# Kernel optimization log

Hardware: AMD Instinct MI355X
Metric: run time of the kernel (lower is better)

## Reference

```python
import jax, jax.numpy as jnp
import numpy as np

B, C, D = 4, 512, 1024
N = 8           # num_experts
DFF = 4096      # GEGLU inner dim; in-projection outputs 2*DFF


def setup_inputs() -> dict:
    key = jax.random.key(0)
    ks = jax.random.split(key, 7)
    hidden_states = jax.random.normal(ks[0], (B, C, D), dtype=jnp.float32)
    # Dispatch mask: one-hot expert assignment per token (top-1 routing).
    assign = jax.random.randint(ks[1], (B, C), 0, N)
    dispatch_mask = jax.nn.one_hot(assign, N, dtype=jnp.float32)        # [B,C,N]
    # Combine mask: same sparsity pattern, scaled by a router probability.
    probs = jax.random.uniform(ks[2], (B, C, 1), dtype=jnp.float32)
    combine_mask = dispatch_mask * probs                                 # [B,C,N]
    s_in = 1.0 / np.sqrt(D)
    s_out = 1.0 / np.sqrt(DFF)
    W_in = jax.random.normal(ks[3], (N, 2 * DFF, D), dtype=jnp.float32) * s_in
    b_in = jax.random.normal(ks[4], (N, 2 * DFF), dtype=jnp.float32) * 0.01
    W_out = jax.random.normal(ks[5], (N, D, DFF), dtype=jnp.float32) * s_out
    b_out = jax.random.normal(ks[6], (N, D), dtype=jnp.float32) * 0.01
    return {"hidden_states": hidden_states, "dispatch_mask": dispatch_mask,
            "combine_mask": combine_mask, "W_in": W_in, "b_in": b_in,
            "W_out": W_out, "b_out": b_out}


def reference(hidden_states, dispatch_mask, combine_mask, W_in, b_in, W_out, b_out):
    # Dispatch: [B,C,D] x [B,C,N] -> [N,B,C,D]
    h = jnp.einsum('bcd,bcn->nbcd', hidden_states, dispatch_mask)
    # Per-expert GEGLU FFN.
    h = jnp.einsum('nbcd,nfd->nbcf', h, W_in) + b_in[:, None, None, :]   # [N,B,C,2*DFF]
    x, gate = jnp.split(h, 2, axis=-1)
    h = x * jax.nn.gelu(gate, approximate=False)                          # torch F.gelu = exact erf
    h = jnp.einsum('nbcd,nfd->nbcf', h, W_out) + b_out[:, None, None, :]  # [N,B,C,D]
    # Combine: [N,B,C,D] x [B,C,N] -> [B,C,D]
    return jnp.einsum('nbcd,bcn->bcd', h, combine_mask)
```

## Files before the change

kernel.cpp:

```cpp
#include <hip/hip_runtime.h>
#include <math.h>

#define NTOK 2048
#define DDIM 1024
#define NEXP 8
#define DFF 4096
#define TWODFF 8192

typedef __attribute__((ext_vector_type(8))) short bf16x8;
typedef __attribute__((ext_vector_type(4))) float f32x4;

__device__ __forceinline__ short f2bf(float f) {
  unsigned u = __builtin_bit_cast(unsigned, f);
  u = (u + 0x7FFFu + ((u >> 16) & 1u)) >> 16;
  return (short)u;
}

__device__ __forceinline__ unsigned pk2(float a, float b) {
  unsigned r;
  asm("v_cvt_pk_bf16_f32 %0, %1, %2" : "=v"(r) : "v"(a), "v"(b));
  return r;
}

__global__ void route_k(const float* __restrict__ disp, const float* __restrict__ comb,
                        int* __restrict__ cnt, int* __restrict__ tokl,
                        float* __restrict__ scale) {
  __shared__ int lcnt[NEXP];
  const int tid = threadIdx.x;
  if (tid < NEXP) lcnt[tid] = 0;
  __syncthreads();
  for (int i = 0; i < 8; ++i) {
    const int t = i * 256 + tid;
    const float* row = disp + (size_t)t * NEXP;
    int e = 0;
#pragma unroll
    for (int n = 1; n < NEXP; ++n) e = (row[n] > row[e]) ? n : e;
    const float p = comb[(size_t)t * NEXP + e];
    const int slot = atomicAdd(&lcnt[e], 1);
    tokl[e * NTOK + slot] = t;
    scale[t] = p;
  }
  __syncthreads();
  if (tid < NEXP) cnt[tid] = lcnt[tid];
}

#define G1_LOAD(aR, bR, k0) do {                                              \
  _Pragma("unroll") for (int i_ = 0; i_ < 4; ++i_) {                          \
    bR[i_] = *(const float4*)(bP[i_] + (k0));                                 \
    aR[i_] = aP[i_] ? *(const float4*)(aP[i_] + (k0))                         \
                    : make_float4(0.f, 0.f, 0.f, 0.f);                        \
  } } while (0)

#define G1_STORE(aR, bR, buf) do {                                            \
  _Pragma("unroll") for (int i_ = 0; i_ < 4; ++i_) {                          \
    const int row_ = i_ * 32 + r0;                                            \
    const int ba_ = (row_ * 64 + (tid & 7) * 8) ^ ((row_ & 7) << 4);          \
    uint2 va_, vb_;                                                           \
    va_.x = pk2(aR[i_].x, aR[i_].y); va_.y = pk2(aR[i_].z, aR[i_].w);         \
    vb_.x = pk2(bR[i_].x, bR[i_].y); vb_.y = pk2(bR[i_].z, bR[i_].w);         \
    *(uint2*)((char*)Al[buf] + ba_) = va_;                                    \
    *(uint2*)((char*)Bl[buf] + ba_) = vb_;                                    \
  } } while (0)

__global__ __launch_bounds__(256, 2) void gemm1_k(
    const float* __restrict__ hid, const float* __restrict__ Win,
    const float* __restrict__ bin, const int* __restrict__ cnt,
    const int* __restrict__ tokl, short* __restrict__ act) {
  const int e = blockIdx.z;
  const int Me = cnt[e];
  const int m0 = blockIdx.y * 128;
  if (m0 >= Me) return;
  const int f0 = blockIdx.x * 64;

  __shared__ short Al[3][128 * 32];
  __shared__ short Bl[3][128 * 32];
  __shared__ int tokids[128];

  const int tid = threadIdx.x;
  if (tid < 128) {
    const int r = m0 + tid;
    tokids[tid] = (r < Me) ? tokl[e * NTOK + r] : -1;
  }
  __syncthreads();

  const int r0 = tid >> 3;
  const int c0 = (tid & 7) * 4;
  const float* aP[4];
  const float* bP[4];
#pragma unroll
  for (int i = 0; i < 4; ++i) {
    const int row = i * 32 + r0;
    const int tk = tokids[row];
    aP[i] = (tk >= 0) ? (hid + (size_t)tk * DDIM + c0) : nullptr;
    const int wr = (row < 64) ? (f0 + row) : (DFF + f0 + (row - 64));
    bP[i] = Win + (size_t)e * TWODFF * DDIM + (size_t)wr * DDIM + c0;
  }

  const int wid = tid >> 6, lane = tid & 63;
  const int wm = (wid >> 1) * 64;
  const int wf = (wid & 1) * 32;
  const int lr = lane & 15;
  const int kbyte = (lane >> 4) * 16;

  f32x4 accx[4][2], accg[4][2];
  const f32x4 zf = {0.f, 0.f, 0.f, 0.f};
#pragma unroll
  for (int a = 0; a < 4; ++a)
#pragma unroll
    for (int b = 0; b < 2; ++b) { accx[a][b] = zf; accg[a][b] = zf; }

  float4 aRa[4], bRa[4], aRb[4], bRb[4];
  G1_LOAD(aRa, bRa, 0);
  G1_STORE(aRa, bRa, 0);
  G1_LOAD(aRa, bRa, 32);
  G1_LOAD(aRb, bRb, 64);

  for (int kt = 0; kt < 32; ++kt) {
    __syncthreads();
    const char* Ab = (const char*)Al[kt % 3];
    const char* Bb = (const char*)Bl[kt % 3];
    bf16x8 a[4], bx[2], bg[2];
#pragma unroll
    for (int fm = 0; fm < 4; ++fm) {
      const int row = wm + fm * 16 + lr;
      a[fm] = *(const bf16x8*)(Ab + ((row * 64 + kbyte) ^ ((row & 7) << 4)));
    }
#pragma unroll
    for (int ff = 0; ff < 2; ++ff) {
      const int rx = wf + ff * 16 + lr;
      bx[ff] = *(const bf16x8*)(Bb + ((rx * 64 + kbyte) ^ ((rx & 7) << 4)));
      const int rg = rx + 64;
      bg[ff] = *(const bf16x8*)(Bb + ((rg * 64 + kbyte) ^ ((rg & 7) << 4)));
    }
#pragma unroll
    for (int fm = 0; fm < 4; ++fm)
#pragma unroll
      for (int ff = 0; ff < 2; ++ff) {
        accx[fm][ff] = __builtin_amdgcn_mfma_f32_16x16x32_bf16(a[fm], bx[ff], accx[fm][ff], 0, 0, 0);
        accg[fm][ff] = __builtin_amdgcn_mfma_f32_16x16x32_bf16(a[fm], bg[ff], accg[fm][ff], 0, 0, 0);
      }
    if (kt < 31) {
      const int wb = (kt + 1) % 3;
      if (kt & 1) {
        G1_STORE(aRb, bRb, wb);
        if (kt < 29) G1_LOAD(aRb, bRb, (kt + 3) * 32);
      } else {
        G1_STORE(aRa, bRa, wb);
        if (kt < 29) G1_LOAD(aRa, bRa, (kt + 3) * 32);
      }
    }
  }

  const int orb = (lane >> 4) * 4;
#pragma unroll
  for (int ff = 0; ff < 2; ++ff) {
    const int fcol = f0 + wf + ff * 16 + lr;
    const float bx_ = bin[e * TWODFF + fcol];
    const float bg_ = bin[e * TWODFF + DFF + fcol];
#pragma unroll
    for (int fm = 0; fm < 4; ++fm)
#pragma unroll
      for (int j = 0; j < 4; ++j) {
        const int row = wm + fm * 16 + orb + j;
        if (m0 + row < Me) {
          const float x = accx[fm][ff][j] + bx_;
          const float g = accg[fm][ff][j] + bg_;
          const float gl = 0.5f * g * (1.f + erff(g * 0.70710678118654752f));
          act[(size_t)tokids[row] * DFF + fcol] = f2bf(x * gl);
        }
      }
  }
}

__global__ __launch_bounds__(256) void gemm2_k(
    const short* __restrict__ act, const float* __restrict__ Wout,
    const float* __restrict__ bout, const int* __restrict__ cnt,
    const int* __restrict__ tokl, const float* __restrict__ scale,
    float* __restrict__ out) {
  const int e = blockIdx.z;
  const int Me = cnt[e];
  const int m0 = blockIdx.y * 128;
  if (m0 >= Me) return;
  const int n0 = blockIdx.x * 64;

  __shared__ short Al[2][128 * 64];
  __shared__ short Bl[2][64 * 64];
  __shared__ int tokids[128];
  __shared__ float pv[128];

  const int tid = threadIdx.x;
  if (tid < 128) {
    const int r = m0 + tid;
    const int tk = (r < Me) ? tokl[e * NTOK + r] : -1;
    tokids[tid] = tk;
    pv[tid] = (tk >= 0) ? scale[tk] : 0.f;
  }
  __syncthreads();

  const int ar0 = tid >> 3;
  const int ac0 = (tid & 7) * 8;
  const short* aP[4];
#pragma unroll
  for (int i = 0; i < 4; ++i) {
    const int row = i * 32 + ar0;
    const int tk = tokids[row];
    aP[i] = (tk >= 0) ? (act + (size_t)tk * DFF + ac0) : nullptr;
  }
  const int br0 = tid >> 4;
  const float* bP[4];
#pragma unroll
  for (int i = 0; i < 4; ++i) {
    const int row = i * 16 + br0;
    bP[i] = Wout + (size_t)e * DDIM * DFF + (size_t)(n0 + row) * DFF + (tid & 15) * 4;
  }

  bf16x8 aR[4];
  float4 bR[4];
  auto load_t = [&](int k0) {
#pragma unroll
    for (int i = 0; i < 4; ++i) bR[i] = *(const float4*)(bP[i] + k0);
    const bf16x8 z = {0, 0, 0, 0, 0, 0, 0, 0};
#pragma unroll
    for (int i = 0; i < 4; ++i) aR[i] = aP[i] ? *(const bf16x8*)(aP[i] + k0) : z;
  };
  auto store_t = [&](int buf) {
#pragma unroll
    for (int i = 0; i < 4; ++i) {
      const int row = i * 32 + ar0;
      const int ba = (row * 128 + (tid & 7) * 16) ^ ((row & 7) << 4);
      *(bf16x8*)((char*)Al[buf] + ba) = aR[i];
    }
#pragma unroll
    for (int i = 0; i < 4; ++i) {
      const int row = i * 16 + br0;
      const int bb = (row * 128 + (tid & 15) * 8) ^ ((row & 7) << 4);
      uint2 vb;
      vb.x = pk2(bR[i].x, bR[i].y); vb.y = pk2(bR[i].z, bR[i].w);
      *(uint2*)((char*)Bl[buf] + bb) = vb;
    }
  };

  const int wid = tid >> 6, lane = tid & 63;
  const int wm = (wid >> 1) * 64;
  const int wn = (wid & 1) * 32;
  const int lr = lane & 15;
  const int lkb = (lane >> 4) * 16;

  f32x4 acc[4][2];
  const f32x4 zf = {0.f, 0.f, 0.f, 0.f};
#pragma unroll
  for (int a = 0; a < 4; ++a) { acc[a][0] = zf; acc[a][1] = zf; }

  load_t(0);
  store_t(0);

  for (int kt = 0; kt < 64; ++kt) {
    if (kt < 63) load_t((kt + 1) * 64);
    __syncthreads();
    const char* Ab = (const char*)Al[kt & 1];
    const char* Bb = (const char*)Bl[kt & 1];
#pragma unroll
    for (int ks = 0; ks < 2; ++ks) {
      bf16x8 a[4], b[2];
      const int kb = ks * 64 + lkb;
#pragma unroll
      for (int fm = 0; fm < 4; ++fm) {
        const int row = wm + fm * 16 + lr;
        a[fm] = *(const bf16x8*)(Ab + ((row * 128 + kb) ^ ((row & 7) << 4)));
      }
#pragma unroll
      for (int ff = 0; ff < 2; ++ff) {
        const int rn = wn + ff * 16 + lr;
        b[ff] = *(const bf16x8*)(Bb + ((rn * 128 + kb) ^ ((rn & 7) << 4)));
      }
#pragma unroll
      for (int fm = 0; fm < 4; ++fm)
#pragma unroll
        for (int ff = 0; ff < 2; ++ff)
          acc[fm][ff] = __builtin_amdgcn_mfma_f32_16x16x32_bf16(a[fm], b[ff], acc[fm][ff], 0, 0, 0);
    }
    if (kt < 63) store_t((kt + 1) & 1);
  }

  const int orb = (lane >> 4) * 4;
#pragma unroll
  for (int ff = 0; ff < 2; ++ff) {
    const int ncol = n0 + wn + ff * 16 + lr;
    const float bo = bout[e * DDIM + ncol];
#pragma unroll
    for (int fm = 0; fm < 4; ++fm)
#pragma unroll
      for (int j = 0; j < 4; ++j) {
        const int row = wm + fm * 16 + orb + j;
        if (m0 + row < Me)
          out[(size_t)tokids[row] * DDIM + ncol] = pv[row] * (acc[fm][ff][j] + bo);
      }
  }
}

extern "C" void kernel_launch(void* const* d_in, const int* in_sizes, int n_in,
                              void* d_out, int out_size, void* d_ws, size_t ws_size,
                              hipStream_t stream) {
  const float* hid = (const float*)d_in[0];
  const float* disp = (const float*)d_in[1];
  const float* comb = (const float*)d_in[2];
  const float* Win = (const float*)d_in[3];
  const float* bin = (const float*)d_in[4];
  const float* Wout = (const float*)d_in[5];
  const float* bout = (const float*)d_in[6];
  float* out = (float*)d_out;

  char* ws = (char*)d_ws;
  int* cnt = (int*)(ws);
  int* tokl = (int*)(ws + 256);
  float* scale = (float*)(ws + 256 + NTOK * NEXP * 4);
  short* act = (short*)(ws + (1 << 17));

  route_k<<<1, 256, 0, stream>>>(disp, comb, cnt, tokl, scale);
  gemm1_k<<<dim3(DFF / 64, 4, NEXP), 256, 0, stream>>>(hid, Win, bin, cnt, tokl, act);
  gemm2_k<<<dim3(DDIM / 64, 4, NEXP), 256, 0, stream>>>(act, Wout, bout, cnt, tokl, scale, out);
}
```

Baseline: 241.5 us.

## Rework GEMM pipelines: double-buffered LDS with two-deep register prefetch

In gemm1 the LDS tiles go from a triple buffer to a double buffer. Global loads for tile kt+2 are now issued right after the barrier, into alternating register sets. In gemm2 the single register stage becomes two alternating register sets that prefetch two tiles ahead, and the kernel gets launch_bounds(256,2). The aim is to hide global latency better, reduce LDS use in gemm1 and raise occupancy in gemm2, at the cost of extra live registers that may cause spills.

```diff
diff --git a/kernel.cpp b/kernel.cpp
--- a/kernel.cpp
+++ b/kernel.cpp
@@ -72,8 +72,8 @@
   if (m0 >= Me) return;
   const int f0 = blockIdx.x * 64;
 
-  __shared__ short Al[3][128 * 32];
-  __shared__ short Bl[3][128 * 32];
+  __shared__ short Al[2][128 * 32];
+  __shared__ short Bl[2][128 * 32];
   __shared__ int tokids[128];
 
   const int tid = threadIdx.x;
@@ -112,13 +112,16 @@
   float4 aRa[4], bRa[4], aRb[4], bRb[4];
   G1_LOAD(aRa, bRa, 0);
   G1_STORE(aRa, bRa, 0);
-  G1_LOAD(aRa, bRa, 32);
-  G1_LOAD(aRb, bRb, 64);
+  G1_LOAD(aRb, bRb, 32);
 
   for (int kt = 0; kt < 32; ++kt) {
     __syncthreads();
-    const char* Ab = (const char*)Al[kt % 3];
-    const char* Bb = (const char*)Bl[kt % 3];
+    if (kt < 30) {
+      if (kt & 1) G1_LOAD(aRb, bRb, (kt + 2) * 32);
+      else        G1_LOAD(aRa, bRa, (kt + 2) * 32);
+    }
+    const char* Ab = (const char*)Al[kt & 1];
+    const char* Bb = (const char*)Bl[kt & 1];
     bf16x8 a[4], bx[2], bg[2];
 #pragma unroll
     for (int fm = 0; fm < 4; ++fm) {
@@ -140,14 +143,8 @@
         accg[fm][ff] = __builtin_amdgcn_mfma_f32_16x16x32_bf16(a[fm], bg[ff], accg[fm][ff], 0, 0, 0);
       }
     if (kt < 31) {
-      const int wb = (kt + 1) % 3;
-      if (kt & 1) {
-        G1_STORE(aRb, bRb, wb);
-        if (kt < 29) G1_LOAD(aRb, bRb, (kt + 3) * 32);
-      } else {
-        G1_STORE(aRa, bRa, wb);
-        if (kt < 29) G1_LOAD(aRa, bRa, (kt + 3) * 32);
-      }
+      if (kt & 1) G1_STORE(aRa, bRa, (kt + 1) & 1);
+      else        G1_STORE(aRb, bRb, (kt + 1) & 1);
     }
   }
 
@@ -172,7 +169,28 @@
   }
 }
 
-__global__ __launch_bounds__(256) void gemm2_k(
+#define G2_LOAD(aR, bR, k0) do {                                              \
+  _Pragma("unroll") for (int i_ = 0; i_ < 4; ++i_)                            \
+    bR[i_] = *(const float4*)(bP[i_] + (k0));                                 \
+  _Pragma("unroll") for (int i_ = 0; i_ < 4; ++i_)                            \
+    aR[i_] = aP[i_] ? *(const bf16x8*)(aP[i_] + (k0)) : zro;                  \
+  } while (0)
+
+#define G2_STORE(aR, bR, buf) do {                                            \
+  _Pragma("unroll") for (int i_ = 0; i_ < 4; ++i_) {                          \
+    const int row_ = i_ * 32 + ar0;                                           \
+    const int ba_ = (row_ * 128 + (tid & 7) * 16) ^ ((row_ & 7) << 4);        \
+    *(bf16x8*)((char*)Al[buf] + ba_) = aR[i_];                                \
+  }                                                                           \
+  _Pragma("unroll") for (int i_ = 0; i_ < 4; ++i_) {                          \
+    const int row_ = i_ * 16 + br0;                                           \
+    const int bb_ = (row_ * 128 + (tid & 15) * 8) ^ ((row_ & 7) << 4);        \
+    uint2 vb_;                                                                \
+    vb_.x = pk2(bR[i_].x, bR[i_].y); vb_.y = pk2(bR[i_].z, bR[i_].w);         \
+    *(uint2*)((char*)Bl[buf] + bb_) = vb_;                                    \
+  } } while (0)
+
+__global__ __launch_bounds__(256, 2) void gemm2_k(
     const short* __restrict__ act, const float* __restrict__ Wout,
     const float* __restrict__ bout, const int* __restrict__ cnt,
     const int* __restrict__ tokl, const float* __restrict__ scale,
@@ -214,32 +232,7 @@
     bP[i] = Wout + (size_t)e * DDIM * DFF + (size_t)(n0 + row) * DFF + (tid & 15) * 4;
   }
 
-  bf16x8 aR[4];
-  float4 bR[4];
-  auto load_t = [&](int k0) {
-#pragma unroll
-    for (int i = 0; i < 4; ++i) bR[i] = *(const float4*)(bP[i] + k0);
-    const bf16x8 z = {0, 0, 0, 0, 0, 0, 0, 0};
-#pragma unroll
-    for (int i = 0; i < 4; ++i) aR[i] = aP[i] ? *(const bf16x8*)(aP[i] + k0) : z;
-  };
-  auto store_t = [&](int buf) {
-#pragma unroll
-    for (int i = 0; i < 4; ++i) {
-      const int row = i * 32 + ar0;
-      const int ba = (row * 128 + (tid & 7) * 16) ^ ((row & 7) << 4);
-      *(bf16x8*)((char*)Al[buf] + ba) = aR[i];
-    }
-#pragma unroll
-    for (int i = 0; i < 4; ++i) {
-      const int row = i * 16 + br0;
-      const int bb = (row * 128 + (tid & 15) * 8) ^ ((row & 7) << 4);
-      uint2 vb;
-      vb.x = pk2(bR[i].x, bR[i].y); vb.y = pk2(bR[i].z, bR[i].w);
-      *(uint2*)((char*)Bl[buf] + bb) = vb;
-    }
-  };
-
+  const bf16x8 zro = {0, 0, 0, 0, 0, 0, 0, 0};
   const int wid = tid >> 6, lane = tid & 63;
   const int wm = (wid >> 1) * 64;
   const int wn = (wid & 1) * 32;
@@ -251,12 +244,18 @@
 #pragma unroll
   for (int a = 0; a < 4; ++a) { acc[a][0] = zf; acc[a][1] = zf; }
 
-  load_t(0);
-  store_t(0);
+  bf16x8 aRa[4], aRb[4];
+  float4 bRa[4], bRb[4];
+  G2_LOAD(aRa, bRa, 0);
+  G2_STORE(aRa, bRa, 0);
+  G2_LOAD(aRb, bRb, 64);
 
   for (int kt = 0; kt < 64; ++kt) {
-    if (kt < 63) load_t((kt + 1) * 64);
     __syncthreads();
+    if (kt < 62) {
+      if (kt & 1) G2_LOAD(aRb, bRb, (kt + 2) * 64);
+      else        G2_LOAD(aRa, bRa, (kt + 2) * 64);
+    }
     const char* Ab = (const char*)Al[kt & 1];
     const char* Bb = (const char*)Bl[kt & 1];
 #pragma unroll
@@ -279,7 +278,10 @@
         for (int ff = 0; ff < 2; ++ff)
           acc[fm][ff] = __builtin_amdgcn_mfma_f32_16x16x32_bf16(a[fm], b[ff], acc[fm][ff], 0, 0, 0);
     }
-    if (kt < 63) store_t((kt + 1) & 1);
+    if (kt < 63) {
+      if (kt & 1) G2_STORE(aRa, bRa, (kt + 1) & 1);
+      else        G2_STORE(aRb, bRb, (kt + 1) & 1);
+    }
   }
 
   const int orb = (lane >> 4) * 4;
```

Result: slower. 260.1 us (+7.7%).

## Switch gemm1 to double-buffered LDS with padded rows and explicit barrier

Applied to the files above, without the earlier changes.

Replaces the triple-buffered, XOR-swizzled LDS staging in the first expert GEMM with two buffers using 80-byte padded rows. Global prefetch is now issued at the start of each iteration, two tiles ahead, and the converted registers are stored after the MFMAs. A custom waitcnt plus s_barrier sits at the end of each iteration instead of __syncthreads at the start. It also drops the min-blocks-per-SM launch bound, which may raise register use and lower occupancy. Padding changes the LDS bank-conflict pattern compared with the swizzle.

```diff
diff --git a/kernel.cpp b/kernel.cpp
--- a/kernel.cpp
+++ b/kernel.cpp
@@ -20,6 +20,11 @@
   unsigned r;
   asm("v_cvt_pk_bf16_f32 %0, %1, %2" : "=v"(r) : "v"(a), "v"(b));
   return r;
+}
+
+__device__ __forceinline__ void ldsbar() {
+  asm volatile("s_waitcnt lgkmcnt(0)" ::: "memory");
+  __builtin_amdgcn_s_barrier();
 }
 
 __global__ void route_k(const float* __restrict__ disp, const float* __restrict__ comb,
@@ -44,25 +49,25 @@
   if (tid < NEXP) cnt[tid] = lcnt[tid];
 }
 
-#define G1_LOAD(aR, bR, k0) do {                                              \
+#define G1_LOAD(sa, sb, k0) do {                                              \
   _Pragma("unroll") for (int i_ = 0; i_ < 4; ++i_) {                          \
-    bR[i_] = *(const float4*)(bP[i_] + (k0));                                 \
-    aR[i_] = aP[i_] ? *(const float4*)(aP[i_] + (k0))                         \
+    sb[i_] = *(const float4*)(bP[i_] + (k0));                                 \
+    sa[i_] = aP[i_] ? *(const float4*)(aP[i_] + (k0))                         \
                     : make_float4(0.f, 0.f, 0.f, 0.f);                        \
   } } while (0)
 
-#define G1_STORE(aR, bR, buf) do {                                            \
+#define G1_STORE(sa, sb, buf) do {                                            \
   _Pragma("unroll") for (int i_ = 0; i_ < 4; ++i_) {                          \
     const int row_ = i_ * 32 + r0;                                            \
-    const int ba_ = (row_ * 64 + (tid & 7) * 8) ^ ((row_ & 7) << 4);          \
+    const int off_ = row_ * 80 + (tid & 7) * 8;                               \
     uint2 va_, vb_;                                                           \
-    va_.x = pk2(aR[i_].x, aR[i_].y); va_.y = pk2(aR[i_].z, aR[i_].w);         \
-    vb_.x = pk2(bR[i_].x, bR[i_].y); vb_.y = pk2(bR[i_].z, bR[i_].w);         \
-    *(uint2*)((char*)Al[buf] + ba_) = va_;                                    \
-    *(uint2*)((char*)Bl[buf] + ba_) = vb_;                                    \
+    va_.x = pk2(sa[i_].x, sa[i_].y); va_.y = pk2(sa[i_].z, sa[i_].w);         \
+    vb_.x = pk2(sb[i_].x, sb[i_].y); vb_.y = pk2(sb[i_].z, sb[i_].w);         \
+    *(uint2*)(Al[buf] + off_) = va_;                                          \
+    *(uint2*)(Bl[buf] + off_) = vb_;                                          \
   } } while (0)
 
-__global__ __launch_bounds__(256, 2) void gemm1_k(
+__global__ __launch_bounds__(256) void gemm1_k(
     const float* __restrict__ hid, const float* __restrict__ Win,
     const float* __restrict__ bin, const int* __restrict__ cnt,
     const int* __restrict__ tokl, short* __restrict__ act) {
@@ -72,8 +77,8 @@
   if (m0 >= Me) return;
   const int f0 = blockIdx.x * 64;
 
-  __shared__ short Al[3][128 * 32];
-  __shared__ short Bl[3][128 * 32];
+  __shared__ char Al[2][128 * 80];
+  __shared__ char Bl[2][128 * 80];
   __shared__ int tokids[128];
 
   const int tid = threadIdx.x;
@@ -100,7 +105,7 @@
   const int wm = (wid >> 1) * 64;
   const int wf = (wid & 1) * 32;
   const int lr = lane & 15;
-  const int kbyte = (lane >> 4) * 16;
+  const int kc = (lane >> 4) * 16;
 
   f32x4 accx[4][2], accg[4][2];
   const f32x4 zf = {0.f, 0.f, 0.f, 0.f};
@@ -109,28 +114,30 @@
 #pragma unroll
     for (int b = 0; b < 2; ++b) { accx[a][b] = zf; accg[a][b] = zf; }
 
-  float4 aRa[4], bRa[4], aRb[4], bRb[4];
-  G1_LOAD(aRa, bRa, 0);
-  G1_STORE(aRa, bRa, 0);
-  G1_LOAD(aRa, bRa, 32);
-  G1_LOAD(aRb, bRb, 64);
+  float4 sAa[4], sBa[4], sAb[4], sBb[4];
+  G1_LOAD(sAa, sBa, 0);
+  G1_STORE(sAa, sBa, 0);
+  G1_LOAD(sAb, sBb, 32);
+  ldsbar();
 
   for (int kt = 0; kt < 32; ++kt) {
-    __syncthreads();
-    const char* Ab = (const char*)Al[kt % 3];
-    const char* Bb = (const char*)Bl[kt % 3];
+    if (kt < 30) {
+      if (kt & 1) G1_LOAD(sAb, sBb, (kt + 2) * 32);
+      else        G1_LOAD(sAa, sBa, (kt + 2) * 32);
+    }
+    const char* Ab = Al[kt & 1];
+    const char* Bb = Bl[kt & 1];
     bf16x8 a[4], bx[2], bg[2];
 #pragma unroll
     for (int fm = 0; fm < 4; ++fm) {
       const int row = wm + fm * 16 + lr;
-      a[fm] = *(const bf16x8*)(Ab + ((row * 64 + kbyte) ^ ((row & 7) << 4)));
+      a[fm] = *(const bf16x8*)(Ab + row * 80 + kc);
     }
 #pragma unroll
     for (int ff = 0; ff < 2; ++ff) {
       const int rx = wf + ff * 16 + lr;
-      bx[ff] = *(const bf16x8*)(Bb + ((rx * 64 + kbyte) ^ ((rx & 7) << 4)));
-      const int rg = rx + 64;
-      bg[ff] = *(const bf16x8*)(Bb + ((rg * 64 + kbyte) ^ ((rg & 7) << 4)));
+      bx[ff] = *(const bf16x8*)(Bb + rx * 80 + kc);
+      bg[ff] = *(const bf16x8*)(Bb + (rx + 64) * 80 + kc);
     }
 #pragma unroll
     for (int fm = 0; fm < 4; ++fm)
@@ -140,15 +147,10 @@
         accg[fm][ff] = __builtin_amdgcn_mfma_f32_16x16x32_bf16(a[fm], bg[ff], accg[fm][ff], 0, 0, 0);
       }
     if (kt < 31) {
-      const int wb = (kt + 1) % 3;
-      if (kt & 1) {
-        G1_STORE(aRb, bRb, wb);
-        if (kt < 29) G1_LOAD(aRb, bRb, (kt + 3) * 32);
-      } else {
-        G1_STORE(aRa, bRa, wb);
-        if (kt < 29) G1_LOAD(aRa, bRa, (kt + 3) * 32);
-      }
-    }
+      if (kt & 1) G1_STORE(sAa, sBa, (kt + 1) & 1);
+      else        G1_STORE(sAb, sBb, (kt + 1) & 1);
+    }
+    ldsbar();
   }
 
   const int orb = (lane >> 4) * 4;
```

Result: slower. 247.8 us (+2.6%).
